# Kernel tuning notes

Hardware: AMD Instinct MI355X
Metric: run time of the kernel (lower is better)

The kernel has to match this reference:

```python
import jax, jax.numpy as jnp
import numpy as np
from jax import lax

EPS = 1e-5

def ste_sign(x):
    # forward-only module: plain sign is fine
    return jnp.sign(x)

def conv2d(x, w, pad):
    # x: NCHW, w: OIHW, stride 1
    return lax.conv_general_dilated(x, w, window_strides=(1, 1),
                                    padding=[(pad, pad), (pad, pad)],
                                    dimension_numbers=('NCHW', 'OIHW', 'NCHW'))

def maxpool2(x):
    # 2x2 max pool, stride 2, VALID (floor) -- matches nn.MaxPool2d(2,2)
    return lax.reduce_window(x, -jnp.inf, lax.max, (1, 1, 2, 2), (1, 1, 2, 2), 'VALID')

def batchnorm(x, gamma, beta):
    # training-mode BN: batch statistics over (N,H,W), biased variance
    mean = jnp.mean(x, axis=(0, 2, 3), keepdims=True)
    var = jnp.var(x, axis=(0, 2, 3), keepdims=True)
    xn = (x - mean) * lax.rsqrt(var + EPS)
    return xn * gamma[None, :, None, None] + beta[None, :, None, None]

def setup_inputs() -> dict:
    key = jax.random.key(0)
    ks = jax.random.split(key, 8)
    def he(k, shape):
        n = shape[2] * shape[3] * shape[0]
        return jax.random.normal(k, shape, jnp.float32) * np.sqrt(2.0 / n)
    x = jax.random.normal(ks[0], (4096, 1, 28, 28), jnp.float32)
    w0 = he(ks[1], (32, 1, 3, 3))
    w1 = he(ks[2], (32, 32, 3, 3))
    w2 = he(ks[3], (32, 32, 3, 3))
    g0 = jnp.ones((32,), jnp.float32); b0 = jnp.zeros((32,), jnp.float32)
    g1 = jnp.ones((32,), jnp.float32); b1 = jnp.zeros((32,), jnp.float32)
    g2 = jnp.ones((32,), jnp.float32); b2 = jnp.zeros((32,), jnp.float32)
    fw = jax.random.normal(ks[4], (10, 288), jnp.float32) * 0.01
    fb = jnp.zeros((10,), jnp.float32)
    return {"x": x, "w0": w0, "g0": g0, "b0": b0, "w1": w1, "g1": g1, "b1": b1,
            "w2": w2, "g2": g2, "b2": b2, "fw": fw, "fb": fb}

def reference(x, w0, g0, b0, w1, g1, b1, w2, g2, b2, fw, fb):
    # block0: fp conv -> pool -> bn (no act)
    h = batchnorm(maxpool2(conv2d(x, w0, 1)), g0, b0)          # [B,32,14,14]
    # block1: binary(1w1a) conv -> pool -> bn + maxpool(shortcut)
    o = batchnorm(maxpool2(conv2d(ste_sign(h), ste_sign(w1), 1)), g1, b1)
    h = o + maxpool2(h)                                         # [B,32,7,7]
    # block2
    o = batchnorm(maxpool2(conv2d(ste_sign(h), ste_sign(w2), 1)), g2, b2)
    h = o + maxpool2(h)                                         # [B,32,3,3]
    h = h.reshape(h.shape[0], -1)                                # [B,288]
    return h @ fw.T + fb                                         # [B,10]
```

## Files before the change

### kernel.cpp

```cpp
#include <hip/hip_runtime.h>
#include <stdint.h>

#define BATCH 4096

typedef float v16f __attribute__((ext_vector_type(16)));
typedef short v8s  __attribute__((ext_vector_type(8)));

__device__ __forceinline__ int sgn8(float v) {
    return (v > 0.f) ? 1 : ((v < 0.f) ? -1 : 0);
}

__global__ __launch_bounds__(448) void k_conv0s(const float* __restrict__ x,
                                                const float* __restrict__ w0,
                                                const float* __restrict__ w1,
                                                const float* __restrict__ w2,
                                                uint16_t* __restrict__ w1f,
                                                uint16_t* __restrict__ w2f,
                                                double* __restrict__ part0) {
    __shared__ float xs[960];
    __shared__ float wl[288];
    __shared__ double rs[448], rq[448];
    int n = blockIdx.x, t = threadIdx.x;

    if (n < 72 && t < 256) {
        int i = n * 256 + t;
        int ii = (i < 9216) ? i : i - 9216;
        const float* w = (i < 9216) ? w1 : w2;
        uint16_t* o = (i < 9216) ? w1f : w2f;
        int j = ii & 7, nn = (ii >> 3) & 31, q2 = (ii >> 8) & 1, kh = (ii >> 9) & 1, tp = ii >> 10;
        int cin = kh * 16 + q2 * 8 + j;
        float v = w[(nn * 32 + cin) * 9 + tp];
        o[ii] = (v > 0.f) ? 0x3F80 : ((v < 0.f) ? 0xBF80 : 0);
    }

    for (int i = t; i < 960; i += 448) xs[i] = 0.f;
    for (int i = t; i < 288; i += 448) wl[i] = w0[i];
    __syncthreads();
    for (int i = t; i < 784; i += 448) {
        int y = i / 28, xx = i - y * 28;
        xs[(y + 1) * 32 + xx + 1] = x[n * 784 + i];
    }
    __syncthreads();
    int c = t & 31, py = t >> 5;
    float wreg[9];
    #pragma unroll
    for (int i = 0; i < 9; ++i) wreg[i] = wl[c * 9 + i];
    const float4* X4 = (const float4*)xs;
    float4 cur0 = X4[(2 * py + 0) * 8];
    float4 cur1 = X4[(2 * py + 1) * 8];
    float4 cur2 = X4[(2 * py + 2) * 8];
    float4 cur3 = X4[(2 * py + 3) * 8];
    double s = 0.0, q = 0.0;
    #pragma unroll
    for (int k = 0; k < 7; ++k) {
        float4 n0 = X4[(2 * py + 0) * 8 + k + 1];
        float4 n1 = X4[(2 * py + 1) * 8 + k + 1];
        float4 n2 = X4[(2 * py + 2) * 8 + k + 1];
        float4 n3 = X4[(2 * py + 3) * 8 + k + 1];
        float a[4][6];
        a[0][0] = cur0.x; a[0][1] = cur0.y; a[0][2] = cur0.z; a[0][3] = cur0.w; a[0][4] = n0.x; a[0][5] = n0.y;
        a[1][0] = cur1.x; a[1][1] = cur1.y; a[1][2] = cur1.z; a[1][3] = cur1.w; a[1][4] = n1.x; a[1][5] = n1.y;
        a[2][0] = cur2.x; a[2][1] = cur2.y; a[2][2] = cur2.z; a[2][3] = cur2.w; a[2][4] = n2.x; a[2][5] = n2.y;
        a[3][0] = cur3.x; a[3][1] = cur3.y; a[3][2] = cur3.z; a[3][3] = cur3.w; a[3][4] = n3.x; a[3][5] = n3.y;
        #pragma unroll
        for (int e = 0; e < 2; ++e) {
            int base = 2 * e;
            float s00 = 0.f, s01 = 0.f, s10 = 0.f, s11 = 0.f;
            #pragma unroll
            for (int ky = 0; ky < 3; ++ky)
            #pragma unroll
            for (int kx = 0; kx < 3; ++kx) {
                float w = wreg[ky * 3 + kx];
                s00 = fmaf(a[ky][base + kx], w, s00);
                s01 = fmaf(a[ky][base + kx + 1], w, s01);
                s10 = fmaf(a[ky + 1][base + kx], w, s10);
                s11 = fmaf(a[ky + 1][base + kx + 1], w, s11);
            }
            float m = fmaxf(fmaxf(s00, s01), fmaxf(s10, s11));
            double v = (double)m;
            s += v; q += v * v;
        }
        cur0 = n0; cur1 = n1; cur2 = n2; cur3 = n3;
    }
    rs[c * 14 + py] = s; rq[c * 14 + py] = q;
    __syncthreads();
    if (t < 32) {
        double S = 0.0, Q = 0.0;
        #pragma unroll
        for (int i = 0; i < 14; ++i) { S += rs[t * 14 + i]; Q += rq[t * 14 + i]; }
        part0[(size_t)t * 4096 + n] = S;
        part0[(size_t)32 * 4096 + (size_t)t * 4096 + n] = Q;
    }
}

__global__ __launch_bounds__(256) void k_finalize(const double* __restrict__ part, int G,
                                                  const float* __restrict__ g,
                                                  const float* __restrict__ b,
                                                  double inv_count, float* __restrict__ ss) {
    int c = blockIdx.x, t = threadIdx.x;
    double s = 0.0, q = 0.0;
    for (int i = t; i < G; i += 256) {
        s += part[(size_t)c * G + i];
        q += part[(size_t)32 * G + (size_t)c * G + i];
    }
    #pragma unroll
    for (int o = 32; o > 0; o >>= 1) { s += __shfl_down(s, o); q += __shfl_down(q, o); }
    __shared__ double rs[4], rq[4];
    int w = t >> 6, l = t & 63;
    if (l == 0) { rs[w] = s; rq[w] = q; }
    __syncthreads();
    if (t == 0) {
        s = rs[0] + rs[1] + rs[2] + rs[3];
        q = rq[0] + rq[1] + rq[2] + rq[3];
        double mean = s * inv_count;
        double var = q * inv_count - mean * mean;
        double sc = (double)g[c] / sqrt(var + 1e-5);
        ss[c] = (float)sc;
        ss[32 + c] = (float)((double)b[c] - mean * sc);
    }
}

__global__ __launch_bounds__(448) void k_bn0r(const float* __restrict__ x,
                                              const float* __restrict__ w0,
                                              const float* __restrict__ ss,
                                              uint32_t* __restrict__ s0b,
                                              float* __restrict__ hp0) {
    __shared__ float xs[960];
    __shared__ float wl[288];
    __shared__ float P[6468];
    int n = blockIdx.x, t = threadIdx.x;
    for (int i = t; i < 960; i += 448) xs[i] = 0.f;
    for (int i = t; i < 288; i += 448) wl[i] = w0[i];
    __syncthreads();
    for (int i = t; i < 784; i += 448) {
        int y = i / 28, xx = i - y * 28;
        xs[(y + 1) * 32 + xx + 1] = x[n * 784 + i];
    }
    __syncthreads();
    int c = t & 31, py = t >> 5;
    float wreg[9];
    #pragma unroll
    for (int i = 0; i < 9; ++i) wreg[i] = wl[c * 9 + i];
    float sc = ss[c], sh = ss[32 + c];
    const float4* X4 = (const float4*)xs;
    float4 cur0 = X4[(2 * py + 0) * 8];
    float4 cur1 = X4[(2 * py + 1) * 8];
    float4 cur2 = X4[(2 * py + 2) * 8];
    float4 cur3 = X4[(2 * py + 3) * 8];
    #pragma unroll
    for (int k = 0; k < 7; ++k) {
        float4 n0 = X4[(2 * py + 0) * 8 + k + 1];
        float4 n1 = X4[(2 * py + 1) * 8 + k + 1];
        float4 n2 = X4[(2 * py + 2) * 8 + k + 1];
        float4 n3 = X4[(2 * py + 3) * 8 + k + 1];
        float a[4][6];
        a[0][0] = cur0.x; a[0][1] = cur0.y; a[0][2] = cur0.z; a[0][3] = cur0.w; a[0][4] = n0.x; a[0][5] = n0.y;
        a[1][0] = cur1.x; a[1][1] = cur1.y; a[1][2] = cur1.z; a[1][3] = cur1.w; a[1][4] = n1.x; a[1][5] = n1.y;
        a[2][0] = cur2.x; a[2][1] = cur2.y; a[2][2] = cur2.z; a[2][3] = cur2.w; a[2][4] = n2.x; a[2][5] = n2.y;
        a[3][0] = cur3.x; a[3][1] = cur3.y; a[3][2] = cur3.z; a[3][3] = cur3.w; a[3][4] = n3.x; a[3][5] = n3.y;
        #pragma unroll
        for (int e = 0; e < 2; ++e) {
            int base = 2 * e;
            float s00 = 0.f, s01 = 0.f, s10 = 0.f, s11 = 0.f;
            #pragma unroll
            for (int ky = 0; ky < 3; ++ky)
            #pragma unroll
            for (int kx = 0; kx < 3; ++kx) {
                float w = wreg[ky * 3 + kx];
                s00 = fmaf(a[ky][base + kx], w, s00);
                s01 = fmaf(a[ky][base + kx + 1], w, s01);
                s10 = fmaf(a[ky + 1][base + kx], w, s10);
                s11 = fmaf(a[ky + 1][base + kx + 1], w, s11);
            }
            float m = fmaxf(fmaxf(s00, s01), fmaxf(s10, s11));
            P[(py * 14 + 2 * k + e) * 33 + c] = fmaf(sc, m, sh);
        }
        cur0 = n0; cur1 = n1; cur2 = n2; cur3 = n3;
    }
    __syncthreads();
    uint32_t* simg = s0b + (size_t)n * 4096;
    for (int i = t; i < 784; i += 448) {
        int pl = i >> 2, qd = i & 3;
        int iy = pl / 14, ix = pl - iy * 14;
        int yy = iy + 1, xx2 = ix + 1;
        int p = yy * 16 + xx2;
        int psw = (xx2 & 3) ^ (yy & 3);
        int g = qd ^ psw;
        const float* Pp = &P[pl * 33 + g * 8];
        uint32_t d[4];
        #pragma unroll
        for (int j = 0; j < 4; ++j) {
            float h0 = Pp[2 * j], h1 = Pp[2 * j + 1];
            uint32_t b0 = (h0 > 0.f) ? 0x3F80u : ((h0 < 0.f) ? 0xBF80u : 0u);
            uint32_t b1 = (h1 > 0.f) ? 0x3F80u : ((h1 < 0.f) ? 0xBF80u : 0u);
            d[j] = b0 | (b1 << 16);
        }
        uint4 v; v.x = d[0]; v.y = d[1]; v.z = d[2]; v.w = d[3];
        *(uint4*)(simg + p * 16 + qd * 4) = v;
    }
    if (t < 240) {
        int e = t >> 2, qd = t & 3;
        int yh, xh;
        if (e < 16)      { yh = 0;      xh = e; }
        else if (e < 32) { yh = 15;     xh = e - 16; }
        else if (e < 46) { yh = e - 31; xh = 0; }
        else             { yh = e - 45; xh = 15; }
        uint4 z; z.x = z.y = z.z = z.w = 0u;
        *(uint4*)(simg + (yh * 16 + xh) * 16 + qd * 4) = z;
    }
    if (t < 196) {
        int pw = t >> 2, oct = t & 3;
        int pyy = pw / 7, pxx = pw - pyy * 7;
        int b00 = ((2 * pyy) * 14 + 2 * pxx) * 33;
        int b01 = b00 + 33;
        int b10 = b00 + 14 * 33;
        int b11 = b10 + 33;
        float out[8];
        #pragma unroll
        for (int k = 0; k < 8; ++k) {
            int cc = oct * 8 + k;
            out[k] = fmaxf(fmaxf(P[b00 + cc], P[b01 + cc]),
                           fmaxf(P[b10 + cc], P[b11 + cc]));
        }
        float4* hd = (float4*)(hp0 + ((size_t)n * 49 + pw) * 32 + oct * 8);
        float4 h0; h0.x = out[0]; h0.y = out[1]; h0.z = out[2]; h0.w = out[3];
        float4 h1; h1.x = out[4]; h1.y = out[5]; h1.z = out[6]; h1.w = out[7];
        hd[0] = h0; hd[1] = h1;
    }
}

__global__ __launch_bounds__(256) void k_conv1m(const uint32_t* __restrict__ s0b,
                                                const uint16_t* __restrict__ w1f,
                                                float* __restrict__ p1,
                                                double* __restrict__ part1) {
    __shared__ uint32_t lds[8192];
    int t = threadIdx.x;
    int n0 = blockIdx.x * 2;
    const uint4* gp = (const uint4*)(s0b + (size_t)n0 * 4096);
    uint4* lp = (uint4*)lds;
    #pragma unroll
    for (int i = 0; i < 8; ++i) lp[t + i * 256] = gp[t + i * 256];
    int lane = t & 63, wv = t >> 6;
    int q = lane >> 5, ncol = lane & 31;
    v8s wfr[18];
    #pragma unroll
    for (int f = 0; f < 18; ++f)
        wfr[f] = *(const v8s*)(w1f + (f * 2 + q) * 256 + ncol * 8);
    __syncthreads();
    int img = wv >> 1, wh = wv & 1;
    int n = n0 + img;
    int ibase = img * 4096;
    int m = lane & 31;
    int quad = m & 3, pwl = m >> 2;
    int dy = quad >> 1, dx = quad & 1;
    double sAcc = 0.0, qAcc = 0.0;
    for (int tile = wh; tile < 7; tile += 2) {
        int pw = tile * 8 + pwl;
        int pwc = min(pw, 48);
        int py = pwc / 7, px = pwc - py * 7;
        int pbase = (2 * py + dy) * 16 + 2 * px + dx;
        v16f acc;
        #pragma unroll
        for (int i = 0; i < 16; ++i) acc[i] = 0.f;
        #pragma unroll
        for (int tp = 0; tp < 9; ++tp) {
            int p = pbase + (tp / 3) * 16 + (tp % 3);
            int psw = (p ^ (p >> 4)) & 3;
            #pragma unroll
            for (int kh = 0; kh < 2; ++kh) {
                int g = kh * 2 + q;
                int idx = ibase + p * 16 + ((g ^ psw) << 2);
                v8s a = *(const v8s*)&lds[idx];
                acc = __builtin_amdgcn_mfma_f32_32x32x16_bf16(a, wfr[tp * 2 + kh], acc, 0, 0, 0);
            }
        }
        #pragma unroll
        for (int g4 = 0; g4 < 4; ++g4) {
            float mx = fmaxf(fmaxf(acc[4 * g4], acc[4 * g4 + 1]),
                             fmaxf(acc[4 * g4 + 2], acc[4 * g4 + 3]));
            int pwo = tile * 8 + 2 * g4 + q;
            if (pwo < 49) {
                p1[((size_t)n * 49 + pwo) * 32 + ncol] = mx;
                double v = (double)mx;
                sAcc += v; qAcc += v * v;
            }
        }
    }
    __syncthreads();
    double* red = (double*)lds;
    red[(wv * 2 + q) * 32 + ncol] = sAcc;
    red[256 + (wv * 2 + q) * 32 + ncol] = qAcc;
    __syncthreads();
    if (t < 32) {
        double S = 0.0, Q = 0.0;
        #pragma unroll
        for (int i = 0; i < 8; ++i) { S += red[i * 32 + t]; Q += red[256 + i * 32 + t]; }
        part1[(size_t)t * 2048 + blockIdx.x] = S;
        part1[(size_t)32 * 2048 + (size_t)t * 2048 + blockIdx.x] = Q;
    }
}

__global__ __launch_bounds__(256) void k_bn1(const float* __restrict__ p1,
                                             const float* __restrict__ hp0,
                                             const float* __restrict__ ss,
                                             uint32_t* __restrict__ s1a,
                                             float* __restrict__ hp1) {
    __shared__ float H[1568];
    int n = blockIdx.x, t = threadIdx.x;
    const float* P = p1 + (size_t)n * 1568;
    const float* Hp = hp0 + (size_t)n * 1568;
    for (int i = t; i < 1568; i += 256) {
        int c = i & 31;
        H[i] = fmaf(ss[64 + c], P[i], ss[96 + c]) + Hp[i];
    }
    __syncthreads();
    uint32_t* sp = s1a + (size_t)n * 1024;
    #pragma unroll
    for (int ii = 0; ii < 4; ++ii) {
        int i = t + ii * 256;
        int p = i >> 4, r = i & 15;
        int y = p >> 3, xq = p & 7;
        uint32_t d = 0u;
        if (y >= 1 && xq >= 1) {
            int pix = (y - 1) * 7 + (xq - 1);
            int sub = r & 3;
            int g = (r >> 2) ^ (p & 3);
            int c0 = ((g << 2) | sub) * 2;
            float h0 = H[pix * 32 + c0];
            float h1 = H[pix * 32 + c0 + 1];
            uint32_t b0 = (h0 > 0.f) ? 0x3F80u : ((h0 < 0.f) ? 0xBF80u : 0u);
            uint32_t b1 = (h1 > 0.f) ? 0x3F80u : ((h1 < 0.f) ? 0xBF80u : 0u);
            d = b0 | (b1 << 16);
        }
        sp[i] = d;
    }
    for (int jj = t; jj < 288; jj += 256) {
        int c = jj / 9, pix = jj - c * 9;
        int r = pix / 3, qq = pix - r * 3;
        float a0 = H[((2 * r) * 7 + 2 * qq) * 32 + c];
        float a1 = H[((2 * r) * 7 + 2 * qq + 1) * 32 + c];
        float a2 = H[((2 * r + 1) * 7 + 2 * qq) * 32 + c];
        float a3 = H[((2 * r + 1) * 7 + 2 * qq + 1) * 32 + c];
        hp1[n * 288 + c * 9 + pix] = fmaxf(fmaxf(a0, a1), fmaxf(a2, a3));
    }
}

__global__ __launch_bounds__(256) void k_conv2m(const uint32_t* __restrict__ s1a,
                                                const uint16_t* __restrict__ w2f,
                                                float* __restrict__ p2,
                                                double* __restrict__ part2) {
    __shared__ uint32_t lds[8192];
    int t = threadIdx.x;
    int n0 = blockIdx.x * 8;
    const uint4* gp4 = (const uint4*)(s1a + (size_t)n0 * 1024);
    uint4* lp = (uint4*)lds;
    #pragma unroll
    for (int i = 0; i < 8; ++i) lp[t + i * 256] = gp4[t + i * 256];
    int lane = t & 63, wv = t >> 6;
    int q = lane >> 5, ncol = lane & 31;
    v8s wfr[18];
    #pragma unroll
    for (int f = 0; f < 18; ++f)
        wfr[f] = *(const v8s*)(w2f + (f * 2 + q) * 256 + ncol * 8);
    __syncthreads();
    int m = lane & 31;
    int quad = m & 3, pwl = m >> 2;
    int dy = quad >> 1, dx = quad & 1;
    double sAcc = 0.0, qAcc = 0.0;
    for (int tile = wv; tile < 9; tile += 4) {
        int pwg = tile * 8 + pwl;
        int img = pwg / 9, pwi = pwg - img * 9;
        int py = pwi / 3, px = pwi - py * 3;
        int pbase = (2 * py + dy) * 8 + 2 * px + dx;
        v16f acc;
        #pragma unroll
        for (int i = 0; i < 16; ++i) acc[i] = 0.f;
        #pragma unroll
        for (int tp = 0; tp < 9; ++tp) {
            int p = pbase + (tp / 3) * 8 + (tp % 3);
            int psw = p & 3;
            #pragma unroll
            for (int kh = 0; kh < 2; ++kh) {
                int g = kh * 2 + q;
                int idx = img * 1024 + p * 16 + ((g ^ psw) << 2);
                v8s a = *(const v8s*)&lds[idx];
                acc = __builtin_amdgcn_mfma_f32_32x32x16_bf16(a, wfr[tp * 2 + kh], acc, 0, 0, 0);
            }
        }
        #pragma unroll
        for (int g4 = 0; g4 < 4; ++g4) {
            float mx = fmaxf(fmaxf(acc[4 * g4], acc[4 * g4 + 1]),
                             fmaxf(acc[4 * g4 + 2], acc[4 * g4 + 3]));
            int pwo = tile * 8 + 2 * g4 + q;
            int oimg = pwo / 9, opwi = pwo - oimg * 9;
            p2[(size_t)(n0 + oimg) * 288 + ncol * 9 + opwi] = mx;
            double v = (double)mx;
            sAcc += v; qAcc += v * v;
        }
    }
    __syncthreads();
    double* red = (double*)lds;
    red[(wv * 2 + q) * 32 + ncol] = sAcc;
    red[256 + (wv * 2 + q) * 32 + ncol] = qAcc;
    __syncthreads();
    if (t < 32) {
        double S = 0.0, Q = 0.0;
        #pragma unroll
        for (int i = 0; i < 8; ++i) { S += red[i * 32 + t]; Q += red[256 + i * 32 + t]; }
        part2[(size_t)t * 512 + blockIdx.x] = S;
        part2[(size_t)32 * 512 + (size_t)t * 512 + blockIdx.x] = Q;
    }
}

__global__ __launch_bounds__(256) void k_fc(const float* __restrict__ p2,
                                            const float* __restrict__ hp1,
                                            const float* __restrict__ ss,
                                            const float* __restrict__ fw,
                                            const float* __restrict__ fb,
                                            float* __restrict__ outv) {
    int wv = threadIdx.x >> 6, l = threadIdx.x & 63;
    int n = blockIdx.x * 4 + wv;
    float acc[10];
    #pragma unroll
    for (int k = 0; k < 10; ++k) acc[k] = 0.f;
    #pragma unroll
    for (int i = 0; i < 5; ++i) {
        int j = l + 64 * i;
        if (j < 288) {
            int c = j / 9;
            float h = fmaf(ss[128 + c], p2[n * 288 + j], ss[160 + c]) + hp1[n * 288 + j];
            #pragma unroll
            for (int k = 0; k < 10; ++k)
                acc[k] = fmaf(h, fw[k * 288 + j], acc[k]);
        }
    }
    #pragma unroll
    for (int k = 0; k < 10; ++k) {
        float s = acc[k];
        #pragma unroll
        for (int o = 32; o > 0; o >>= 1) s += __shfl_down(s, o);
        if (l == 0) outv[n * 10 + k] = s + fb[k];
    }
}

extern "C" void kernel_launch(void* const* d_in, const int* in_sizes, int n_in,
                              void* d_out, int out_size, void* d_ws, size_t ws_size,
                              hipStream_t stream) {
    (void)in_sizes; (void)n_in; (void)out_size; (void)ws_size;
    const float* x  = (const float*)d_in[0];
    const float* w0 = (const float*)d_in[1];
    const float* g0 = (const float*)d_in[2];
    const float* b0 = (const float*)d_in[3];
    const float* w1 = (const float*)d_in[4];
    const float* g1 = (const float*)d_in[5];
    const float* b1 = (const float*)d_in[6];
    const float* w2 = (const float*)d_in[7];
    const float* g2 = (const float*)d_in[8];
    const float* b2 = (const float*)d_in[9];
    const float* fw = (const float*)d_in[10];
    const float* fb = (const float*)d_in[11];
    float* outv = (float*)d_out;
    char* ws = (char*)d_ws;

    float*     ss    = (float*)(ws + 1024);
    uint16_t*  w1f   = (uint16_t*)(ws + 2048);
    uint16_t*  w2f   = (uint16_t*)(ws + 38912);
    float*     p1    = (float*)(ws + 76800);
    float*     hp1   = (float*)(ws + 32582656);
    float*     p2    = (float*)(ws + 37301248);
    uint32_t*  s0b   = (uint32_t*)(ws + 42019840);
    uint32_t*  s1a   = (uint32_t*)(ws + 42019840);
    double*    part0 = (double*)(ws + 109128704);
    double*    part1 = (double*)(ws + 111225856);
    double*    part2 = (double*)(ws + 112274432);
    float*     hp0   = (float*)(ws + 128527360);

    k_conv0s<<<BATCH, 448, 0, stream>>>(x, w0, w1, w2, w1f, w2f, part0);
    k_finalize<<<32, 256, 0, stream>>>(part0, 4096, g0, b0, 1.0 / (BATCH * 196.0), ss);
    k_bn0r<<<BATCH, 448, 0, stream>>>(x, w0, ss, s0b, hp0);

    k_conv1m<<<BATCH / 2, 256, 0, stream>>>(s0b, w1f, p1, part1);
    k_finalize<<<32, 256, 0, stream>>>(part1, 2048, g1, b1, 1.0 / (BATCH * 49.0), ss + 64);
    k_bn1<<<BATCH, 256, 0, stream>>>(p1, hp0, ss, s1a, hp1);

    k_conv2m<<<BATCH / 8, 256, 0, stream>>>(s1a, w2f, p2, part2);
    k_finalize<<<32, 256, 0, stream>>>(part2, 512, g2, b2, 1.0 / (BATCH * 9.0), ss + 128);

    k_fc<<<BATCH / 4, 256, 0, stream>>>(p2, hp1, ss, fw, fb, outv);
}
```

Baseline: 211.1 us.

## Fuse all stages into one cooperative persistent kernel with grid syncs

Replaces the chain of nine kernel launches (conv0 stats, finalize, bn0, conv1, finalize, bn1, conv2, finalize, fc) with a single cooperative kernel of 512 blocks that loops over images and uses grid.sync between stages. This removes launch overhead and inter-kernel gaps, at the cost of lower per-stage parallelism (256 threads per block instead of 448, persistent loops) and finalize phases where only 32 blocks work while the rest wait at the barrier. The original launch sequence is kept as a fallback if the cooperative launch fails.

```diff
diff --git a/kernel.cpp b/kernel.cpp
--- a/kernel.cpp
+++ b/kernel.cpp
@@ -1,5 +1,8 @@
 #include <hip/hip_runtime.h>
+#include <hip/hip_cooperative_groups.h>
 #include <stdint.h>
+
+namespace cg = cooperative_groups;
 
 #define BATCH 4096
 
@@ -8,6 +11,469 @@
 
 __device__ __forceinline__ int sgn8(float v) {
     return (v > 0.f) ? 1 : ((v < 0.f) ? -1 : 0);
+}
+
+__device__ __forceinline__ void finalize_dev(const double* __restrict__ part, int G,
+                                             const float* __restrict__ g,
+                                             const float* __restrict__ b,
+                                             double inv_count, float* __restrict__ ssout,
+                                             int c, int t, char* smem) {
+    double s = 0.0, q = 0.0;
+    for (int i = t; i < G; i += 256) {
+        s += part[(size_t)c * G + i];
+        q += part[(size_t)32 * G + (size_t)c * G + i];
+    }
+    #pragma unroll
+    for (int o = 32; o > 0; o >>= 1) { s += __shfl_down(s, o); q += __shfl_down(q, o); }
+    double* rs = (double*)smem;
+    double* rq = rs + 4;
+    int w = t >> 6, l = t & 63;
+    if (l == 0) { rs[w] = s; rq[w] = q; }
+    __syncthreads();
+    if (t == 0) {
+        s = rs[0] + rs[1] + rs[2] + rs[3];
+        q = rq[0] + rq[1] + rq[2] + rq[3];
+        double mean = s * inv_count;
+        double var = q * inv_count - mean * mean;
+        double sc = (double)g[c] / sqrt(var + 1e-5);
+        ssout[c] = (float)sc;
+        ssout[32 + c] = (float)((double)b[c] - mean * sc);
+    }
+    __syncthreads();
+}
+
+__global__ __launch_bounds__(256, 2) void k_mega(
+    const float* __restrict__ x,  const float* __restrict__ w0,
+    const float* __restrict__ w1, const float* __restrict__ w2,
+    const float* __restrict__ g0, const float* __restrict__ b0,
+    const float* __restrict__ g1, const float* __restrict__ b1,
+    const float* __restrict__ g2, const float* __restrict__ b2,
+    const float* __restrict__ fw, const float* __restrict__ fb,
+    uint16_t* __restrict__ w1f, uint16_t* __restrict__ w2f,
+    float* __restrict__ ss, float* __restrict__ p1,
+    float* __restrict__ hp1, float* __restrict__ p2,
+    uint32_t* __restrict__ s0b, double* __restrict__ part0,
+    double* __restrict__ part1, double* __restrict__ part2,
+    float* __restrict__ hp0, float* __restrict__ outv)
+{
+    __shared__ __align__(16) char smem[32768];
+    cg::grid_group grid = cg::this_grid();
+    int t = threadIdx.x, blk = blockIdx.x;
+    int lane = t & 63, wv = t >> 6;
+
+    {
+        int i = blk * 256 + t;
+        if (i < 18432) {
+            int ii = (i < 9216) ? i : i - 9216;
+            const float* w = (i < 9216) ? w1 : w2;
+            uint16_t* o = (i < 9216) ? w1f : w2f;
+            int j = ii & 7, nn = (ii >> 3) & 31, q2 = (ii >> 8) & 1, kh = (ii >> 9) & 1, tp = ii >> 10;
+            int cin = kh * 16 + q2 * 8 + j;
+            float v = w[(nn * 32 + cin) * 9 + tp];
+            o[ii] = (v > 0.f) ? 0x3F80 : ((v < 0.f) ? 0xBF80 : 0);
+        }
+    }
+
+    {
+        float* xs = (float*)smem;
+        float* wl = xs + 960;
+        double* rs = (double*)(smem + 5120);
+        double* rq = rs + 448;
+        int c = t & 31, py0 = t >> 5;
+        for (int rep = 0; rep < 8; ++rep) {
+            int n = blk + rep * 512;
+            for (int i = t; i < 960; i += 256) xs[i] = 0.f;
+            if (rep == 0) for (int i = t; i < 288; i += 256) wl[i] = w0[i];
+            __syncthreads();
+            for (int i = t; i < 784; i += 256) {
+                int y = i / 28, xx = i - y * 28;
+                xs[(y + 1) * 32 + xx + 1] = x[n * 784 + i];
+            }
+            __syncthreads();
+            float wreg[9];
+            #pragma unroll
+            for (int i = 0; i < 9; ++i) wreg[i] = wl[c * 9 + i];
+            const float4* X4 = (const float4*)xs;
+            for (int py = py0; py < 14; py += 8) {
+                float4 cur0 = X4[(2 * py + 0) * 8];
+                float4 cur1 = X4[(2 * py + 1) * 8];
+                float4 cur2 = X4[(2 * py + 2) * 8];
+                float4 cur3 = X4[(2 * py + 3) * 8];
+                double s = 0.0, q = 0.0;
+                #pragma unroll
+                for (int k = 0; k < 7; ++k) {
+                    float4 n0 = X4[(2 * py + 0) * 8 + k + 1];
+                    float4 n1 = X4[(2 * py + 1) * 8 + k + 1];
+                    float4 n2 = X4[(2 * py + 2) * 8 + k + 1];
+                    float4 n3 = X4[(2 * py + 3) * 8 + k + 1];
+                    float a[4][6];
+                    a[0][0] = cur0.x; a[0][1] = cur0.y; a[0][2] = cur0.z; a[0][3] = cur0.w; a[0][4] = n0.x; a[0][5] = n0.y;
+                    a[1][0] = cur1.x; a[1][1] = cur1.y; a[1][2] = cur1.z; a[1][3] = cur1.w; a[1][4] = n1.x; a[1][5] = n1.y;
+                    a[2][0] = cur2.x; a[2][1] = cur2.y; a[2][2] = cur2.z; a[2][3] = cur2.w; a[2][4] = n2.x; a[2][5] = n2.y;
+                    a[3][0] = cur3.x; a[3][1] = cur3.y; a[3][2] = cur3.z; a[3][3] = cur3.w; a[3][4] = n3.x; a[3][5] = n3.y;
+                    #pragma unroll
+                    for (int e = 0; e < 2; ++e) {
+                        int base = 2 * e;
+                        float s00 = 0.f, s01 = 0.f, s10 = 0.f, s11 = 0.f;
+                        #pragma unroll
+                        for (int ky = 0; ky < 3; ++ky)
+                        #pragma unroll
+                        for (int kx = 0; kx < 3; ++kx) {
+                            float w = wreg[ky * 3 + kx];
+                            s00 = fmaf(a[ky][base + kx], w, s00);
+                            s01 = fmaf(a[ky][base + kx + 1], w, s01);
+                            s10 = fmaf(a[ky + 1][base + kx], w, s10);
+                            s11 = fmaf(a[ky + 1][base + kx + 1], w, s11);
+                        }
+                        float m = fmaxf(fmaxf(s00, s01), fmaxf(s10, s11));
+                        double v = (double)m;
+                        s += v; q += v * v;
+                    }
+                    cur0 = n0; cur1 = n1; cur2 = n2; cur3 = n3;
+                }
+                rs[c * 14 + py] = s; rq[c * 14 + py] = q;
+            }
+            __syncthreads();
+            if (t < 32) {
+                double S = 0.0, Q = 0.0;
+                #pragma unroll
+                for (int i = 0; i < 14; ++i) { S += rs[t * 14 + i]; Q += rq[t * 14 + i]; }
+                part0[(size_t)t * 4096 + n] = S;
+                part0[(size_t)32 * 4096 + (size_t)t * 4096 + n] = Q;
+            }
+            __syncthreads();
+        }
+    }
+    grid.sync();
+
+    if (blk < 32) finalize_dev(part0, 4096, g0, b0, 1.0 / (4096.0 * 196.0), ss, blk, t, smem);
+    grid.sync();
+
+    {
+        float* xs = (float*)smem;
+        float* wl = xs + 960;
+        float* P  = (float*)(smem + 5120);
+        int c = t & 31, py0 = t >> 5;
+        float scv = ss[c], shv = ss[32 + c];
+        for (int rep = 0; rep < 8; ++rep) {
+            int n = blk + rep * 512;
+            for (int i = t; i < 960; i += 256) xs[i] = 0.f;
+            if (rep == 0) for (int i = t; i < 288; i += 256) wl[i] = w0[i];
+            __syncthreads();
+            for (int i = t; i < 784; i += 256) {
+                int y = i / 28, xx = i - y * 28;
+                xs[(y + 1) * 32 + xx + 1] = x[n * 784 + i];
+            }
+            __syncthreads();
+            float wreg[9];
+            #pragma unroll
+            for (int i = 0; i < 9; ++i) wreg[i] = wl[c * 9 + i];
+            const float4* X4 = (const float4*)xs;
+            for (int py = py0; py < 14; py += 8) {
+                float4 cur0 = X4[(2 * py + 0) * 8];
+                float4 cur1 = X4[(2 * py + 1) * 8];
+                float4 cur2 = X4[(2 * py + 2) * 8];
+                float4 cur3 = X4[(2 * py + 3) * 8];
+                #pragma unroll
+                for (int k = 0; k < 7; ++k) {
+                    float4 n0 = X4[(2 * py + 0) * 8 + k + 1];
+                    float4 n1 = X4[(2 * py + 1) * 8 + k + 1];
+                    float4 n2 = X4[(2 * py + 2) * 8 + k + 1];
+                    float4 n3 = X4[(2 * py + 3) * 8 + k + 1];
+                    float a[4][6];
+                    a[0][0] = cur0.x; a[0][1] = cur0.y; a[0][2] = cur0.z; a[0][3] = cur0.w; a[0][4] = n0.x; a[0][5] = n0.y;
+                    a[1][0] = cur1.x; a[1][1] = cur1.y; a[1][2] = cur1.z; a[1][3] = cur1.w; a[1][4] = n1.x; a[1][5] = n1.y;
+                    a[2][0] = cur2.x; a[2][1] = cur2.y; a[2][2] = cur2.z; a[2][3] = cur2.w; a[2][4] = n2.x; a[2][5] = n2.y;
+                    a[3][0] = cur3.x; a[3][1] = cur3.y; a[3][2] = cur3.z; a[3][3] = cur3.w; a[3][4] = n3.x; a[3][5] = n3.y;
+                    #pragma unroll
+                    for (int e = 0; e < 2; ++e) {
+                        int base = 2 * e;
+                        float s00 = 0.f, s01 = 0.f, s10 = 0.f, s11 = 0.f;
+                        #pragma unroll
+                        for (int ky = 0; ky < 3; ++ky)
+                        #pragma unroll
+                        for (int kx = 0; kx < 3; ++kx) {
+                            float w = wreg[ky * 3 + kx];
+                            s00 = fmaf(a[ky][base + kx], w, s00);
+                            s01 = fmaf(a[ky][base + kx + 1], w, s01);
+                            s10 = fmaf(a[ky + 1][base + kx], w, s10);
+                            s11 = fmaf(a[ky + 1][base + kx + 1], w, s11);
+                        }
+                        float m = fmaxf(fmaxf(s00, s01), fmaxf(s10, s11));
+                        P[(py * 14 + 2 * k + e) * 33 + c] = fmaf(scv, m, shv);
+                    }
+                    cur0 = n0; cur1 = n1; cur2 = n2; cur3 = n3;
+                }
+            }
+            __syncthreads();
+            uint32_t* simg = s0b + (size_t)n * 4096;
+            for (int i = t; i < 784; i += 256) {
+                int pl = i >> 2, qd = i & 3;
+                int iy = pl / 14, ix = pl - iy * 14;
+                int yy = iy + 1, xx2 = ix + 1;
+                int p = yy * 16 + xx2;
+                int psw = (xx2 & 3) ^ (yy & 3);
+                int g = qd ^ psw;
+                const float* Pp = &P[pl * 33 + g * 8];
+                uint32_t d[4];
+                #pragma unroll
+                for (int j = 0; j < 4; ++j) {
+                    float h0 = Pp[2 * j], h1 = Pp[2 * j + 1];
+                    uint32_t b0v = (h0 > 0.f) ? 0x3F80u : ((h0 < 0.f) ? 0xBF80u : 0u);
+                    uint32_t b1v = (h1 > 0.f) ? 0x3F80u : ((h1 < 0.f) ? 0xBF80u : 0u);
+                    d[j] = b0v | (b1v << 16);
+                }
+                uint4 v; v.x = d[0]; v.y = d[1]; v.z = d[2]; v.w = d[3];
+                *(uint4*)(simg + p * 16 + qd * 4) = v;
+            }
+            if (t < 240) {
+                int e = t >> 2, qd = t & 3;
+                int yh, xh;
+                if (e < 16)      { yh = 0;      xh = e; }
+                else if (e < 32) { yh = 15;     xh = e - 16; }
+                else if (e < 46) { yh = e - 31; xh = 0; }
+                else             { yh = e - 45; xh = 15; }
+                uint4 z; z.x = z.y = z.z = z.w = 0u;
+                *(uint4*)(simg + (yh * 16 + xh) * 16 + qd * 4) = z;
+            }
+            if (t < 196) {
+                int pw = t >> 2, oct = t & 3;
+                int pyy = pw / 7, pxx = pw - pyy * 7;
+                int b00 = ((2 * pyy) * 14 + 2 * pxx) * 33;
+                int b01 = b00 + 33;
+                int b10 = b00 + 14 * 33;
+                int b11 = b10 + 33;
+                float out[8];
+                #pragma unroll
+                for (int k = 0; k < 8; ++k) {
+                    int cc = oct * 8 + k;
+                    out[k] = fmaxf(fmaxf(P[b00 + cc], P[b01 + cc]),
+                                   fmaxf(P[b10 + cc], P[b11 + cc]));
+                }
+                float4* hd = (float4*)(hp0 + ((size_t)n * 49 + pw) * 32 + oct * 8);
+                float4 h0; h0.x = out[0]; h0.y = out[1]; h0.z = out[2]; h0.w = out[3];
+                float4 h1; h1.x = out[4]; h1.y = out[5]; h1.z = out[6]; h1.w = out[7];
+                hd[0] = h0; hd[1] = h1;
+            }
+            __syncthreads();
+        }
+    }
+    grid.sync();
+
+    {
+        uint32_t* lds = (uint32_t*)smem;
+        int q = lane >> 5, ncol = lane & 31;
+        v8s wfr[18];
+        #pragma unroll
+        for (int f = 0; f < 18; ++f)
+            wfr[f] = *(const v8s*)(w1f + (f * 2 + q) * 256 + ncol * 8);
+        int img = wv >> 1, wh = wv & 1;
+        int m = lane & 31;
+        int quad = m & 3, pwl = m >> 2;
+        int dy = quad >> 1, dx = quad & 1;
+        for (int rep = 0; rep < 4; ++rep) {
+            int pr = blk + rep * 512;
+            int n0 = pr * 2;
+            const uint4* gp = (const uint4*)(s0b + (size_t)n0 * 4096);
+            uint4* lp = (uint4*)lds;
+            #pragma unroll
+            for (int i = 0; i < 8; ++i) lp[t + i * 256] = gp[t + i * 256];
+            __syncthreads();
+            int n = n0 + img;
+            int ibase = img * 4096;
+            double sAcc = 0.0, qAcc = 0.0;
+            for (int tile = wh; tile < 7; tile += 2) {
+                int pw = tile * 8 + pwl;
+                int pwc = min(pw, 48);
+                int py = pwc / 7, px = pwc - py * 7;
+                int pbase = (2 * py + dy) * 16 + 2 * px + dx;
+                v16f acc;
+                #pragma unroll
+                for (int i = 0; i < 16; ++i) acc[i] = 0.f;
+                #pragma unroll
+                for (int tp = 0; tp < 9; ++tp) {
+                    int p = pbase + (tp / 3) * 16 + (tp % 3);
+                    int psw = (p ^ (p >> 4)) & 3;
+                    #pragma unroll
+                    for (int kh = 0; kh < 2; ++kh) {
+                        int g = kh * 2 + q;
+                        int idx = ibase + p * 16 + ((g ^ psw) << 2);
+                        v8s a = *(const v8s*)&lds[idx];
+                        acc = __builtin_amdgcn_mfma_f32_32x32x16_bf16(a, wfr[tp * 2 + kh], acc, 0, 0, 0);
+                    }
+                }
+                #pragma unroll
+                for (int g4 = 0; g4 < 4; ++g4) {
+                    float mx = fmaxf(fmaxf(acc[4 * g4], acc[4 * g4 + 1]),
+                                     fmaxf(acc[4 * g4 + 2], acc[4 * g4 + 3]));
+                    int pwo = tile * 8 + 2 * g4 + q;
+                    if (pwo < 49) {
+                        p1[((size_t)n * 49 + pwo) * 32 + ncol] = mx;
+                        double v = (double)mx;
+                        sAcc += v; qAcc += v * v;
+                    }
+                }
+            }
+            __syncthreads();
+            double* red = (double*)smem;
+            red[(wv * 2 + q) * 32 + ncol] = sAcc;
+            red[256 + (wv * 2 + q) * 32 + ncol] = qAcc;
+            __syncthreads();
+            if (t < 32) {
+                double S = 0.0, Q = 0.0;
+                #pragma unroll
+                for (int i = 0; i < 8; ++i) { S += red[i * 32 + t]; Q += red[256 + i * 32 + t]; }
+                part1[(size_t)t * 2048 + pr] = S;
+                part1[(size_t)32 * 2048 + (size_t)t * 2048 + pr] = Q;
+            }
+            __syncthreads();
+        }
+    }
+    grid.sync();
+
+    if (blk < 32) finalize_dev(part1, 2048, g1, b1, 1.0 / (4096.0 * 49.0), ss + 64, blk, t, smem);
+    grid.sync();
+
+    {
+        float* H = (float*)smem;
+        uint32_t* s1a = s0b;
+        for (int rep = 0; rep < 8; ++rep) {
+            int n = blk + rep * 512;
+            const float* P = p1 + (size_t)n * 1568;
+            const float* Hp = hp0 + (size_t)n * 1568;
+            for (int i = t; i < 1568; i += 256) {
+                int c = i & 31;
+                H[i] = fmaf(ss[64 + c], P[i], ss[96 + c]) + Hp[i];
+            }
+            __syncthreads();
+            uint32_t* sp = s1a + (size_t)n * 1024;
+            #pragma unroll
+            for (int ii = 0; ii < 4; ++ii) {
+                int i = t + ii * 256;
+                int p = i >> 4, r = i & 15;
+                int y = p >> 3, xq = p & 7;
+                uint32_t d = 0u;
+                if (y >= 1 && xq >= 1) {
+                    int pix = (y - 1) * 7 + (xq - 1);
+                    int sub = r & 3;
+                    int g = (r >> 2) ^ (p & 3);
+                    int c0 = ((g << 2) | sub) * 2;
+                    float h0 = H[pix * 32 + c0];
+                    float h1 = H[pix * 32 + c0 + 1];
+                    uint32_t b0v = (h0 > 0.f) ? 0x3F80u : ((h0 < 0.f) ? 0xBF80u : 0u);
+                    uint32_t b1v = (h1 > 0.f) ? 0x3F80u : ((h1 < 0.f) ? 0xBF80u : 0u);
+                    d = b0v | (b1v << 16);
+                }
+                sp[i] = d;
+            }
+            for (int jj = t; jj < 288; jj += 256) {
+                int c = jj / 9, pix = jj - c * 9;
+                int r = pix / 3, qq = pix - r * 3;
+                float a0 = H[((2 * r) * 7 + 2 * qq) * 32 + c];
+                float a1 = H[((2 * r) * 7 + 2 * qq + 1) * 32 + c];
+                float a2 = H[((2 * r + 1) * 7 + 2 * qq) * 32 + c];
+                float a3 = H[((2 * r + 1) * 7 + 2 * qq + 1) * 32 + c];
+                hp1[n * 288 + c * 9 + pix] = fmaxf(fmaxf(a0, a1), fmaxf(a2, a3));
+            }
+            __syncthreads();
+        }
+    }
+    grid.sync();
+
+    {
+        uint32_t* lds = (uint32_t*)smem;
+        uint32_t* s1a = s0b;
+        int n0 = blk * 8;
+        const uint4* gp4 = (const uint4*)(s1a + (size_t)n0 * 1024);
+        uint4* lp = (uint4*)lds;
+        #pragma unroll
+        for (int i = 0; i < 8; ++i) lp[t + i * 256] = gp4[t + i * 256];
+        int q = lane >> 5, ncol = lane & 31;
+        v8s wfr[18];
+        #pragma unroll
+        for (int f = 0; f < 18; ++f)
+            wfr[f] = *(const v8s*)(w2f + (f * 2 + q) * 256 + ncol * 8);
+        __syncthreads();
+        int m = lane & 31;
+        int quad = m & 3, pwl = m >> 2;
+        int dy = quad >> 1, dx = quad & 1;
+        double sAcc = 0.0, qAcc = 0.0;
+        for (int tile = wv; tile < 9; tile += 4) {
+            int pwg = tile * 8 + pwl;
+            int img = pwg / 9, pwi = pwg - img * 9;
+            int py = pwi / 3, px = pwi - py * 3;
+            int pbase = (2 * py + dy) * 8 + 2 * px + dx;
+            v16f acc;
+            #pragma unroll
+            for (int i = 0; i < 16; ++i) acc[i] = 0.f;
+            #pragma unroll
+            for (int tp = 0; tp < 9; ++tp) {
+                int p = pbase + (tp / 3) * 8 + (tp % 3);
+                int psw = p & 3;
+                #pragma unroll
+                for (int kh = 0; kh < 2; ++kh) {
+                    int g = kh * 2 + q;
+                    int idx = img * 1024 + p * 16 + ((g ^ psw) << 2);
+                    v8s a = *(const v8s*)&lds[idx];
+                    acc = __builtin_amdgcn_mfma_f32_32x32x16_bf16(a, wfr[tp * 2 + kh], acc, 0, 0, 0);
+                }
+            }
+            #pragma unroll
+            for (int g4 = 0; g4 < 4; ++g4) {
+                float mx = fmaxf(fmaxf(acc[4 * g4], acc[4 * g4 + 1]),
+                                 fmaxf(acc[4 * g4 + 2], acc[4 * g4 + 3]));
+                int pwo = tile * 8 + 2 * g4 + q;
+                int oimg = pwo / 9, opwi = pwo - oimg * 9;
+                p2[(size_t)(n0 + oimg) * 288 + ncol * 9 + opwi] = mx;
+                double v = (double)mx;
+                sAcc += v; qAcc += v * v;
+            }
+        }
+        __syncthreads();
+        double* red = (double*)smem;
+        red[(wv * 2 + q) * 32 + ncol] = sAcc;
+        red[256 + (wv * 2 + q) * 32 + ncol] = qAcc;
+        __syncthreads();
+        if (t < 32) {
+            double S = 0.0, Q = 0.0;
+            #pragma unroll
+            for (int i = 0; i < 8; ++i) { S += red[i * 32 + t]; Q += red[256 + i * 32 + t]; }
+            part2[(size_t)t * 512 + blk] = S;
+            part2[(size_t)32 * 512 + (size_t)t * 512 + blk] = Q;
+        }
+    }
+    grid.sync();
+
+    if (blk < 32) finalize_dev(part2, 512, g2, b2, 1.0 / (4096.0 * 9.0), ss + 128, blk, t, smem);
+    grid.sync();
+
+    {
+        for (int rep = 0; rep < 2; ++rep) {
+            int n = (blk * 2 + rep) * 4 + wv;
+            int l = lane;
+            float acc[10];
+            #pragma unroll
+            for (int k = 0; k < 10; ++k) acc[k] = 0.f;
+            #pragma unroll
+            for (int i = 0; i < 5; ++i) {
+                int j = l + 64 * i;
+                if (j < 288) {
+                    int c = j / 9;
+                    float h = fmaf(ss[128 + c], p2[n * 288 + j], ss[160 + c]) + hp1[n * 288 + j];
+                    #pragma unroll
+                    for (int k = 0; k < 10; ++k)
+                        acc[k] = fmaf(h, fw[k * 288 + j], acc[k]);
+                }
+            }
+            #pragma unroll
+            for (int k = 0; k < 10; ++k) {
+                float s = acc[k];
+                #pragma unroll
+                for (int o = 32; o > 0; o >>= 1) s += __shfl_down(s, o);
+                if (l == 0) outv[n * 10 + k] = s + fb[k];
+            }
+        }
+    }
 }
 
 __global__ __launch_bounds__(448) void k_conv0s(const float* __restrict__ x,
@@ -21,7 +487,6 @@
     __shared__ float wl[288];
     __shared__ double rs[448], rq[448];
     int n = blockIdx.x, t = threadIdx.x;
-
     if (n < 72 && t < 256) {
         int i = n * 256 + t;
         int ii = (i < 9216) ? i : i - 9216;
@@ -32,7 +497,6 @@
         float v = w[(nn * 32 + cin) * 9 + tp];
         o[ii] = (v > 0.f) ? 0x3F80 : ((v < 0.f) ? 0xBF80 : 0);
     }
-
     for (int i = t; i < 960; i += 448) xs[i] = 0.f;
     for (int i = t; i < 288; i += 448) wl[i] = w0[i];
     __syncthreads();
@@ -97,27 +561,8 @@
                                                   const float* __restrict__ g,
                                                   const float* __restrict__ b,
                                                   double inv_count, float* __restrict__ ss) {
-    int c = blockIdx.x, t = threadIdx.x;
-    double s = 0.0, q = 0.0;
-    for (int i = t; i < G; i += 256) {
-        s += part[(size_t)c * G + i];
-        q += part[(size_t)32 * G + (size_t)c * G + i];
-    }
-    #pragma unroll
-    for (int o = 32; o > 0; o >>= 1) { s += __shfl_down(s, o); q += __shfl_down(q, o); }
-    __shared__ double rs[4], rq[4];
-    int w = t >> 6, l = t & 63;
-    if (l == 0) { rs[w] = s; rq[w] = q; }
-    __syncthreads();
-    if (t == 0) {
-        s = rs[0] + rs[1] + rs[2] + rs[3];
-        q = rq[0] + rq[1] + rq[2] + rq[3];
-        double mean = s * inv_count;
-        double var = q * inv_count - mean * mean;
-        double sc = (double)g[c] / sqrt(var + 1e-5);
-        ss[c] = (float)sc;
-        ss[32 + c] = (float)((double)b[c] - mean * sc);
-    }
+    __shared__ __align__(16) char smem[64];
+    finalize_dev(part, G, g, b, inv_count, ss, blockIdx.x, threadIdx.x, smem);
 }
 
 __global__ __launch_bounds__(448) void k_bn0r(const float* __restrict__ x,
@@ -469,22 +914,31 @@
     float*     hp1   = (float*)(ws + 32582656);
     float*     p2    = (float*)(ws + 37301248);
     uint32_t*  s0b   = (uint32_t*)(ws + 42019840);
-    uint32_t*  s1a   = (uint32_t*)(ws + 42019840);
     double*    part0 = (double*)(ws + 109128704);
     double*    part1 = (double*)(ws + 111225856);
     double*    part2 = (double*)(ws + 112274432);
     float*     hp0   = (float*)(ws + 128527360);
 
-    k_conv0s<<<BATCH, 448, 0, stream>>>(x, w0, w1, w2, w1f, w2f, part0);
-    k_finalize<<<32, 256, 0, stream>>>(part0, 4096, g0, b0, 1.0 / (BATCH * 196.0), ss);
-    k_bn0r<<<BATCH, 448, 0, stream>>>(x, w0, ss, s0b, hp0);
-
-    k_conv1m<<<BATCH / 2, 256, 0, stream>>>(s0b, w1f, p1, part1);
-    k_finalize<<<32, 256, 0, stream>>>(part1, 2048, g1, b1, 1.0 / (BATCH * 49.0), ss + 64);
-    k_bn1<<<BATCH, 256, 0, stream>>>(p1, hp0, ss, s1a, hp1);
-
-    k_conv2m<<<BATCH / 8, 256, 0, stream>>>(s1a, w2f, p2, part2);
-    k_finalize<<<32, 256, 0, stream>>>(part2, 512, g2, b2, 1.0 / (BATCH * 9.0), ss + 128);
-
-    k_fc<<<BATCH / 4, 256, 0, stream>>>(p2, hp1, ss, fw, fb, outv);
-}
+    void* kargs[] = {
+        (void*)&x, (void*)&w0, (void*)&w1, (void*)&w2,
+        (void*)&g0, (void*)&b0, (void*)&g1, (void*)&b1,
+        (void*)&g2, (void*)&b2, (void*)&fw, (void*)&fb,
+        (void*)&w1f, (void*)&w2f, (void*)&ss, (void*)&p1,
+        (void*)&hp1, (void*)&p2, (void*)&s0b,
+        (void*)&part0, (void*)&part1, (void*)&part2, (void*)&hp0,
+        (void*)&outv
+    };
+    hipError_t err = hipLaunchCooperativeKernel((void*)k_mega, dim3(512), dim3(256),
+                                                kargs, 0, stream);
+    if (err != hipSuccess) {
+        k_conv0s<<<BATCH, 448, 0, stream>>>(x, w0, w1, w2, w1f, w2f, part0);
+        k_finalize<<<32, 256, 0, stream>>>(part0, 4096, g0, b0, 1.0 / (BATCH * 196.0), ss);
+        k_bn0r<<<BATCH, 448, 0, stream>>>(x, w0, ss, s0b, hp0);
+        k_conv1m<<<BATCH / 2, 256, 0, stream>>>(s0b, w1f, p1, part1);
+        k_finalize<<<32, 256, 0, stream>>>(part1, 2048, g1, b1, 1.0 / (BATCH * 49.0), ss + 64);
+        k_bn1<<<BATCH, 256, 0, stream>>>(p1, hp0, ss, s0b, hp1);
+        k_conv2m<<<BATCH / 8, 256, 0, stream>>>(s0b, w2f, p2, part2);
+        k_finalize<<<32, 256, 0, stream>>>(part2, 512, g2, b2, 1.0 / (BATCH * 9.0), ss + 128);
+        k_fc<<<BATCH / 4, 256, 0, stream>>>(p2, hp1, ss, fw, fb, outv);
+    }
+}
```

New measurement: 700.7 us. 232% more time.
